# Optimization experiments

Measured on AMD Instinct MI355X. Metric: run time of the kernel, lower is better.

## Reference

```python
import jax, jax.numpy as jnp
import numpy as np

N_NODES = 50000
N_EDGES = 1600000
IN_CH = 128
HID = 64
HEADS = 2
OUT_CH2 = HID // 8  # 8
OUT_FC = 1
N_GRAPHS = 64
NEG_SLOPE = 0.2


def setup_inputs() -> dict:
    key = jax.random.key(0)
    ks = jax.random.split(key, 12)
    x = jax.random.normal(ks[0], (N_NODES, IN_CH), dtype=jnp.float32)
    edge_index = jax.random.randint(ks[1], (2, N_EDGES), 0, N_NODES, dtype=jnp.int32)
    batch = jnp.sort(jax.random.randint(ks[2], (N_NODES,), 0, N_GRAPHS, dtype=jnp.int32))
    s = lambda fan: 1.0 / np.sqrt(fan)
    W1 = jax.random.normal(ks[3], (IN_CH, HEADS * HID), dtype=jnp.float32) * s(IN_CH)
    att_src1 = jax.random.normal(ks[4], (HEADS, HID), dtype=jnp.float32) * s(HID)
    att_dst1 = jax.random.normal(ks[5], (HEADS, HID), dtype=jnp.float32) * s(HID)
    b1 = jnp.zeros((HEADS * HID,), dtype=jnp.float32)
    W2 = jax.random.normal(ks[6], (HEADS * HID, OUT_CH2), dtype=jnp.float32) * s(HEADS * HID)
    att_src2 = jax.random.normal(ks[7], (1, OUT_CH2), dtype=jnp.float32) * s(OUT_CH2)
    att_dst2 = jax.random.normal(ks[8], (1, OUT_CH2), dtype=jnp.float32) * s(OUT_CH2)
    b2 = jnp.zeros((OUT_CH2,), dtype=jnp.float32)
    fcW = jax.random.normal(ks[9], (OUT_CH2, OUT_FC), dtype=jnp.float32) * s(OUT_CH2)
    fcb = jnp.zeros((OUT_FC,), dtype=jnp.float32)
    return {"x": x, "edge_index": edge_index, "batch": batch,
            "W1": W1, "att_src1": att_src1, "att_dst1": att_dst1, "b1": b1,
            "W2": W2, "att_src2": att_src2, "att_dst2": att_dst2, "b2": b2,
            "fcW": fcW, "fcb": fcb}


def gat_conv(x, edge_index, W, att_src, att_dst, bias, heads, out_ch):
    """PyG GATConv (concat=True, add_self_loops=True, negative_slope=0.2, eval mode)."""
    n = x.shape[0]
    loop = jnp.arange(n, dtype=edge_index.dtype)
    src = jnp.concatenate([edge_index[0], loop])
    dst = jnp.concatenate([edge_index[1], loop])
    h = (x @ W).reshape(n, heads, out_ch)                 # [N,H,C]
    a_src = jnp.sum(h * att_src[None], axis=-1)           # [N,H]
    a_dst = jnp.sum(h * att_dst[None], axis=-1)           # [N,H]
    logits = jax.nn.leaky_relu(a_src[src] + a_dst[dst], NEG_SLOPE)  # [E,H]
    m = jax.ops.segment_max(logits, dst, num_segments=n)  # segment softmax over dst
    e = jnp.exp(logits - m[dst])
    denom = jax.ops.segment_sum(e, dst, num_segments=n)
    alpha = e / denom[dst]                                # [E,H]
    msg = h[src] * alpha[:, :, None]                      # [E,H,C]
    out = jax.ops.segment_sum(msg, dst, num_segments=n)   # [N,H,C]
    return out.reshape(n, heads * out_ch) + bias


def reference(x, edge_index, batch, W1, att_src1, att_dst1, b1,
              W2, att_src2, att_dst2, b2, fcW, fcb):
    h = gat_conv(x, edge_index, W1, att_src1, att_dst1, b1, HEADS, HID)
    h = jax.nn.relu(h)
    h = gat_conv(h, edge_index, W2, att_src2, att_dst2, b2, 1, OUT_CH2)
    h = jax.nn.relu(h)
    # global_mean_pool over graphs
    sums = jax.ops.segment_sum(h, batch, num_segments=N_GRAPHS)
    cnts = jax.ops.segment_sum(jnp.ones((h.shape[0],), h.dtype), batch, num_segments=N_GRAPHS)
    pooled = sums / jnp.maximum(cnts, 1.0)[:, None]       # [G, OUT_CH2]
    y = pooled @ fcW + fcb
    y = 2.0 * jax.nn.sigmoid(y) - 1.0
    return y.squeeze(-1)                                  # [G]
```

## Files before the change

kernel.cpp:

```cpp
#include <hip/hip_runtime.h>
#include <math.h>

#define MAXD 96

__device__ __forceinline__ float lrelu(float v){ return v >= 0.f ? v : 0.2f * v; }

__device__ __forceinline__ unsigned short f2bf(float f){
  unsigned u = __float_as_uint(f);
  return (unsigned short)((u + 0x7fffu + ((u >> 16) & 1u)) >> 16);
}

__global__ void countK(const int* __restrict__ dstA, int E, int ET,
                       int* __restrict__ deg8, int* __restrict__ erank, int n){
  int e = blockIdx.x * blockDim.x + threadIdx.x;
  if (e >= ET) return;
  int d = (e < E) ? dstA[e] : (e - E);
  int r = blockIdx.x & 7;
  erank[e] = atomicAdd(&deg8[r * n + d], 1);
}

__global__ void scanA(int* __restrict__ deg8, int* __restrict__ excl,
                      int* __restrict__ part, int n){
  __shared__ int s[256];
  int t = threadIdx.x;
  int i = blockIdx.x * 256 + t;
  int v = 0;
  if (i < n){
    int run = 0;
    #pragma unroll
    for (int r = 0; r < 8; ++r){
      int c = deg8[r * n + i];
      deg8[r * n + i] = run;
      run += c;
    }
    v = run;
  }
  s[t] = v;
  __syncthreads();
  for (int o = 1; o < 256; o <<= 1){
    int tv = (t >= o) ? s[t - o] : 0;
    __syncthreads();
    s[t] += tv;
    __syncthreads();
  }
  if (i < n) excl[i] = s[t] - v;
  if (t == 255) part[blockIdx.x] = s[t];
}

__global__ void scanB(int* __restrict__ part, int nb){
  __shared__ int s[256];
  int t = threadIdx.x;
  int v = (t < nb) ? part[t] : 0;
  s[t] = v;
  __syncthreads();
  for (int o = 1; o < 256; o <<= 1){
    int tv = (t >= o) ? s[t - o] : 0;
    __syncthreads();
    s[t] += tv;
    __syncthreads();
  }
  if (t < nb) part[t] = s[t] - v;
}

__global__ void scanC(int* __restrict__ off, const int* __restrict__ part, int n, int ET){
  int i = blockIdx.x * 256 + threadIdx.x;
  if (i < n) off[i] += part[blockIdx.x];
  if (i == 0) off[n] = ET;
}

__global__ void scatterK(const int* __restrict__ srcA, const int* __restrict__ dstA, int E, int ET,
                         const int* __restrict__ off, const int* __restrict__ deg8,
                         const int* __restrict__ erank, int* __restrict__ csrc, int n){
  int e = blockIdx.x * blockDim.x + threadIdx.x;
  if (e >= ET) return;
  int s, d;
  if (e < E){ s = srcA[e]; d = dstA[e]; } else { s = e - E; d = s; }
  int r = (e >> 8) & 7;
  csrc[off[d] + deg8[r * n + d] + erank[e]] = s;
}

__global__ __launch_bounds__(256, 2) void gemm1(const float* __restrict__ x, const float* __restrict__ W1,
    const float* __restrict__ attS, const float* __restrict__ attD,
    unsigned short* __restrict__ h1b, float* __restrict__ a1s, float* __restrict__ a1d, int nN){
  __shared__ float4 Ws4[128][32];
  __shared__ float4 xs4[32][32];
  int t = threadIdx.x;
  const float4* Wg = reinterpret_cast<const float4*>(W1);
  #pragma unroll
  for (int i = 0; i < 16; ++i){
    int idx = t + i * 256;
    Ws4[idx >> 5][idx & 31] = Wg[idx];
  }
  int n0 = blockIdx.x * 32;
  const float4* xg = reinterpret_cast<const float4*>(x);
  #pragma unroll
  for (int i = 0; i < 4; ++i){
    int idx = t + i * 256;
    int r = idx >> 5, c = idx & 31;
    int gn = n0 + r; if (gn >= nN) gn = nN - 1;
    xs4[r][c ^ (r & 7)] = xg[(size_t)gn * 32 + c];
  }
  __syncthreads();
  int cb = t & 15, nl = t >> 4;
  int cb2 = cb * 2;
  int c0 = cb * 8;
  int sw = nl & 7;
  float4 accA0 = make_float4(0.f,0.f,0.f,0.f), accA1 = accA0;
  float4 accB0 = accA0, accB1 = accA0;
  #pragma unroll 2
  for (int k4 = 0; k4 < 32; ++k4){
    float4 xv0 = xs4[nl][k4 ^ sw];
    float4 xv1 = xs4[nl + 16][k4 ^ sw];
    float xa[4] = {xv0.x, xv0.y, xv0.z, xv0.w};
    float xb[4] = {xv1.x, xv1.y, xv1.z, xv1.w};
    #pragma unroll
    for (int j = 0; j < 4; ++j){
      float4 wA = Ws4[4 * k4 + j][cb2];
      float4 wB = Ws4[4 * k4 + j][cb2 + 1];
      accA0.x = fmaf(xa[j], wA.x, accA0.x);
      accA0.y = fmaf(xa[j], wA.y, accA0.y);
      accA0.z = fmaf(xa[j], wA.z, accA0.z);
      accA0.w = fmaf(xa[j], wA.w, accA0.w);
      accA1.x = fmaf(xa[j], wB.x, accA1.x);
      accA1.y = fmaf(xa[j], wB.y, accA1.y);
      accA1.z = fmaf(xa[j], wB.z, accA1.z);
      accA1.w = fmaf(xa[j], wB.w, accA1.w);
      accB0.x = fmaf(xb[j], wA.x, accB0.x);
      accB0.y = fmaf(xb[j], wA.y, accB0.y);
      accB0.z = fmaf(xb[j], wA.z, accB0.z);
      accB0.w = fmaf(xb[j], wA.w, accB0.w);
      accB1.x = fmaf(xb[j], wB.x, accB1.x);
      accB1.y = fmaf(xb[j], wB.y, accB1.y);
      accB1.z = fmaf(xb[j], wB.z, accB1.z);
      accB1.w = fmaf(xb[j], wB.w, accB1.w);
    }
  }
  float4 as0 = *reinterpret_cast<const float4*>(attS + c0);
  float4 as1 = *reinterpret_cast<const float4*>(attS + c0 + 4);
  float4 ad0 = *reinterpret_cast<const float4*>(attD + c0);
  float4 ad1 = *reinterpret_cast<const float4*>(attD + c0 + 4);
  #pragma unroll
  for (int j = 0; j < 2; ++j){
    int n = n0 + nl + j * 16;
    if (n >= nN) continue;
    float4 h0 = j ? accB0 : accA0;
    float4 h1v = j ? accB1 : accA1;
    uint4 pk;
    pk.x = (unsigned)f2bf(h0.x)  | ((unsigned)f2bf(h0.y)  << 16);
    pk.y = (unsigned)f2bf(h0.z)  | ((unsigned)f2bf(h0.w)  << 16);
    pk.z = (unsigned)f2bf(h1v.x) | ((unsigned)f2bf(h1v.y) << 16);
    pk.w = (unsigned)f2bf(h1v.z) | ((unsigned)f2bf(h1v.w) << 16);
    *reinterpret_cast<uint4*>(h1b + (size_t)n * 128 + c0) = pk;
    float s = h0.x*as0.x + h0.y*as0.y + h0.z*as0.z + h0.w*as0.w
            + h1v.x*as1.x + h1v.y*as1.y + h1v.z*as1.z + h1v.w*as1.w;
    float d = h0.x*ad0.x + h0.y*ad0.y + h0.z*ad0.z + h0.w*ad0.w
            + h1v.x*ad1.x + h1v.y*ad1.y + h1v.z*ad1.z + h1v.w*ad1.w;
    s += __shfl_xor(s, 1); s += __shfl_xor(s, 2); s += __shfl_xor(s, 4);
    d += __shfl_xor(d, 1); d += __shfl_xor(d, 2); d += __shfl_xor(d, 4);
    if ((cb & 7) == 0){
      int head = cb >> 3;
      a1s[n * 2 + head] = s;
      a1d[n * 2 + head] = d;
    }
  }
}

__global__ __launch_bounds__(256) void agg1(const int* __restrict__ off, const int* __restrict__ csrc,
    const float* __restrict__ a1s, const float* __restrict__ a1d,
    const unsigned short* __restrict__ h1b, const float* __restrict__ b1,
    const float* __restrict__ W2, const float* __restrict__ attS2, const float* __restrict__ attD2,
    float* __restrict__ h2, float* __restrict__ a2s, float* __restrict__ a2d, int nN){
  __shared__ float al[4][MAXD][2];
  __shared__ int   sidx[4][MAXD];
  int t = threadIdx.x;
  int w = t >> 6, lane = t & 63;
  int n = blockIdx.x * 4 + w;
  if (n >= nN) return;
  int start = off[n], end = off[n + 1];
  int deg = end - start;
  int degc = deg < MAXD ? deg : MAXD;
  float ad0 = a1d[2 * n], ad1 = a1d[2 * n + 1];
  float ls0 = 0.f, ls1 = 0.f;
  for (int i = lane; i < degc; i += 64){
    int s = csrc[start + i];
    sidx[w][i] = s;
    float2 as = *reinterpret_cast<const float2*>(a1s + 2 * s);
    float e0 = __expf(lrelu(as.x + ad0));
    float e1 = __expf(lrelu(as.y + ad1));
    al[w][i][0] = e0; al[w][i][1] = e1;
    ls0 += e0; ls1 += e1;
  }
  #pragma unroll
  for (int o = 32; o > 0; o >>= 1){
    ls0 += __shfl_xor(ls0, o);
    ls1 += __shfl_xor(ls1, o);
  }
  float d0 = ls0, d1 = ls1;
  int c4 = (lane & 31) * 4;
  int h = c4 >> 6;
  int sub = lane >> 5;
  float4 acc = make_float4(0.f, 0.f, 0.f, 0.f);
  #pragma unroll 8
  for (int k = 0; k < degc; k += 2){
    int e = k + sub;
    bool ok = e < degc;
    int ee = ok ? e : degc - 1;
    int s = sidx[w][ee];
    float wgt = ok ? al[w][ee][h] : 0.f;
    uint2 v = *reinterpret_cast<const uint2*>(h1b + (size_t)s * 128 + c4);
    acc.x = fmaf(wgt, __uint_as_float(v.x << 16),         acc.x);
    acc.y = fmaf(wgt, __uint_as_float(v.x & 0xffff0000u), acc.y);
    acc.z = fmaf(wgt, __uint_as_float(v.y << 16),         acc.z);
    acc.w = fmaf(wgt, __uint_as_float(v.y & 0xffff0000u), acc.w);
  }
  acc.x += __shfl_xor(acc.x, 32);
  acc.y += __shfl_xor(acc.y, 32);
  acc.z += __shfl_xor(acc.z, 32);
  acc.w += __shfl_xor(acc.w, 32);
  float inv = 1.f / (h ? d1 : d0);
  float4 bb = *reinterpret_cast<const float4*>(b1 + c4);
  float oj[4];
  oj[0] = fmaxf(fmaf(acc.x, inv, bb.x), 0.f);
  oj[1] = fmaxf(fmaf(acc.y, inv, bb.y), 0.f);
  oj[2] = fmaxf(fmaf(acc.z, inv, bb.z), 0.f);
  oj[3] = fmaxf(fmaf(acc.w, inv, bb.w), 0.f);
  const float4* W2v = reinterpret_cast<const float4*>(W2);
  float p8[8] = {0.f,0.f,0.f,0.f,0.f,0.f,0.f,0.f};
  #pragma unroll
  for (int j = 0; j < 4; ++j){
    float4 wlo = W2v[(c4 + j) * 2];
    float4 whi = W2v[(c4 + j) * 2 + 1];
    p8[0] = fmaf(oj[j], wlo.x, p8[0]); p8[1] = fmaf(oj[j], wlo.y, p8[1]);
    p8[2] = fmaf(oj[j], wlo.z, p8[2]); p8[3] = fmaf(oj[j], wlo.w, p8[3]);
    p8[4] = fmaf(oj[j], whi.x, p8[4]); p8[5] = fmaf(oj[j], whi.y, p8[5]);
    p8[6] = fmaf(oj[j], whi.z, p8[6]); p8[7] = fmaf(oj[j], whi.w, p8[7]);
  }
  #pragma unroll
  for (int o = 16; o > 0; o >>= 1){
    #pragma unroll
    for (int cc = 0; cc < 8; ++cc) p8[cc] += __shfl_xor(p8[cc], o);
  }
  if (lane == 0){
    *reinterpret_cast<float4*>(h2 + (size_t)n * 8)     = make_float4(p8[0], p8[1], p8[2], p8[3]);
    *reinterpret_cast<float4*>(h2 + (size_t)n * 8 + 4) = make_float4(p8[4], p8[5], p8[6], p8[7]);
    float s2 = 0.f, dd2 = 0.f;
    #pragma unroll
    for (int cc = 0; cc < 8; ++cc){
      s2  = fmaf(p8[cc], attS2[cc], s2);
      dd2 = fmaf(p8[cc], attD2[cc], dd2);
    }
    a2s[n] = s2; a2d[n] = dd2;
  }
}

__global__ __launch_bounds__(256) void agg2(const int* __restrict__ off, const int* __restrict__ csrc,
    const float* __restrict__ a2s, const float* __restrict__ a2d,
    const float* __restrict__ h2, const float* __restrict__ b2, float* __restrict__ out2, int nN){
  __shared__ float al[4][MAXD];
  __shared__ int sidx[4][MAXD];
  int t = threadIdx.x;
  int w = t >> 6, lane = t & 63;
  int n = blockIdx.x * 4 + w;
  if (n >= nN) return;
  int start = off[n], end = off[n + 1];
  int deg = end - start, degc = deg < MAXD ? deg : MAXD;
  float ad = a2d[n];
  float ls = 0.f;
  for (int i = lane; i < degc; i += 64){
    int s = csrc[start + i];
    sidx[w][i] = s;
    float e = __expf(lrelu(a2s[s] + ad));
    al[w][i] = e;
    ls += e;
  }
  #pragma unroll
  for (int o = 32; o > 0; o >>= 1) ls += __shfl_xor(ls, o);
  float dv = ls;
  int c = lane & 7, eb = lane >> 3;
  float acc = 0.f;
  #pragma unroll 4
  for (int k = 0; k < degc; k += 8){
    int e = k + eb;
    bool ok = e < degc;
    int ee = ok ? e : degc - 1;
    float wgt = ok ? al[w][ee] : 0.f;
    acc = fmaf(wgt, h2[(size_t)sidx[w][ee] * 8 + c], acc);
  }
  acc += __shfl_xor(acc, 8);
  acc += __shfl_xor(acc, 16);
  acc += __shfl_xor(acc, 32);
  if (lane < 8) out2[(size_t)n * 8 + lane] = fmaxf(acc / dv + b2[lane], 0.f);
}

__global__ __launch_bounds__(256) void poolFC(const float* __restrict__ out2,
    const int* __restrict__ batch, const float* __restrict__ fcW,
    const float* __restrict__ fcb, float* __restrict__ out, int nN){
  __shared__ float red[256];
  int g = blockIdx.x;
  int lo = 0, hi = nN;
  while (lo < hi){ int m = (lo + hi) >> 1; if (batch[m] < g) lo = m + 1; else hi = m; }
  int s = lo;
  hi = nN;
  while (lo < hi){ int m = (lo + hi) >> 1; if (batch[m] < g + 1) lo = m + 1; else hi = m; }
  int e = lo;
  int t = threadIdx.x;
  int c = t & 7, row = t >> 3;
  float acc = 0.f;
  for (int i = s + row; i < e; i += 32) acc += out2[(size_t)i * 8 + c];
  red[t] = acc;
  __syncthreads();
  for (int o = 128; o >= 8; o >>= 1){
    if (t < o) red[t] += red[t + o];
    __syncthreads();
  }
  if (t == 0){
    float cc = fmaxf((float)(e - s), 1.0f);
    float y = fcb[0];
    #pragma unroll
    for (int c2 = 0; c2 < 8; ++c2) y += (red[c2] / cc) * fcW[c2];
    out[g] = 2.f / (1.f + expf(-y)) - 1.f;
  }
}

extern "C" void kernel_launch(void* const* d_in, const int* in_sizes, int n_in,
                              void* d_out, int out_size, void* d_ws, size_t ws_size,
                              hipStream_t stream){
  const float* x    = (const float*)d_in[0];
  const int*   ei   = (const int*)d_in[1];
  const int*   batch= (const int*)d_in[2];
  const float* W1   = (const float*)d_in[3];
  const float* aS1  = (const float*)d_in[4];
  const float* aD1  = (const float*)d_in[5];
  const float* b1   = (const float*)d_in[6];
  const float* W2   = (const float*)d_in[7];
  const float* aS2  = (const float*)d_in[8];
  const float* aD2  = (const float*)d_in[9];
  const float* b2   = (const float*)d_in[10];
  const float* fcW  = (const float*)d_in[11];
  const float* fcb  = (const float*)d_in[12];
  float* out = (float*)d_out;

  const int N  = in_sizes[0] / 128;
  const int E  = in_sizes[1] / 2;
  const int ET = E + N;
  const int G  = 64;

  const int* eiSrc = ei;
  const int* eiDst = ei + E;

  char* w = (char*)d_ws;
  size_t o = 0;
  auto alloc = [&](size_t bytes)->char*{
    o = (o + 255) & ~(size_t)255;
    char* p = w + o;
    o += bytes;
    return p;
  };
  int*   deg8   = (int*)  alloc((size_t)N * 8 * 4);
  size_t zbytes = (size_t)N * 8 * 4;
  int*   csrOff = (int*)  alloc((size_t)(N + 1) * 4);
  int*   part   = (int*)  alloc(256 * 4);
  int*   erank  = (int*)  alloc((size_t)ET * 4);
  int*   csrc   = (int*)  alloc((size_t)ET * 4);
  unsigned short* h1b = (unsigned short*)alloc((size_t)N * 128 * 2);
  float* a1s    = (float*)alloc((size_t)N * 2 * 4);
  float* a1d    = (float*)alloc((size_t)N * 2 * 4);
  float* h2     = (float*)alloc((size_t)N * 8 * 4);
  float* a2s    = (float*)alloc((size_t)N * 4);
  float* a2d    = (float*)alloc((size_t)N * 4);
  float* out2   = (float*)alloc((size_t)N * 8 * 4);
  (void)ws_size; (void)n_in; (void)out_size;

  hipMemsetAsync(deg8, 0, zbytes, stream);

  int ebl = (ET + 255) / 256;
  int nbl = (N + 255) / 256;

  countK  <<<ebl, 256, 0, stream>>>(eiDst, E, ET, deg8, erank, N);
  scanA   <<<nbl, 256, 0, stream>>>(deg8, csrOff, part, N);
  scanB   <<<1,   256, 0, stream>>>(part, nbl);
  scanC   <<<nbl, 256, 0, stream>>>(csrOff, part, N, ET);
  scatterK<<<ebl, 256, 0, stream>>>(eiSrc, eiDst, E, ET, csrOff, deg8, erank, csrc, N);

  gemm1<<<(N + 31) / 32, 256, 0, stream>>>(x, W1, aS1, aD1, h1b, a1s, a1d, N);
  agg1 <<<(N + 3) / 4, 256, 0, stream>>>(csrOff, csrc, a1s, a1d, h1b, b1, W2, aS2, aD2, h2, a2s, a2d, N);
  agg2 <<<(N + 3) / 4, 256, 0, stream>>>(csrOff, csrc, a2s, a2d, h2, b2, out2, N);
  poolFC<<<G, 256, 0, stream>>>(out2, batch, fcW, fcb, out, N);
}
```

Measured before the change: 264.3 us.

## Fuse CSR build into one cooperative kernel with register-held edge ranks

Replaces the memset, count, three scan kernels and scatter with a single cooperative-launched kernel that separates phases with grid-wide syncs. Each thread keeps its edges' destinations and atomic ranks in registers, so the erank array no longer has to be written and reread through global memory. The aggregation loop's unroll factor is also raised. The trade is several grid barriers and a fixed grid size in place of separate launches.

```diff
diff --git a/kernel.cpp b/kernel.cpp
--- a/kernel.cpp
+++ b/kernel.cpp
@@ -1,7 +1,12 @@
 #include <hip/hip_runtime.h>
+#include <hip/hip_cooperative_groups.h>
 #include <math.h>
 
+namespace cg = cooperative_groups;
+
 #define MAXD 96
+#define CSRB 1024
+#define EPT  7
 
 __device__ __forceinline__ float lrelu(float v){ return v >= 0.f ? v : 0.2f * v; }
 
@@ -10,73 +15,83 @@
   return (unsigned short)((u + 0x7fffu + ((u >> 16) & 1u)) >> 16);
 }
 
-__global__ void countK(const int* __restrict__ dstA, int E, int ET,
-                       int* __restrict__ deg8, int* __restrict__ erank, int n){
-  int e = blockIdx.x * blockDim.x + threadIdx.x;
-  if (e >= ET) return;
-  int d = (e < E) ? dstA[e] : (e - E);
-  int r = blockIdx.x & 7;
-  erank[e] = atomicAdd(&deg8[r * n + d], 1);
-}
-
-__global__ void scanA(int* __restrict__ deg8, int* __restrict__ excl,
-                      int* __restrict__ part, int n){
+__global__ __launch_bounds__(256, 4) void csrK(const int* __restrict__ srcA, const int* __restrict__ dstA,
+                                               int E, int ET, int nN,
+                                               int* __restrict__ deg8, int* __restrict__ csrOff,
+                                               int* __restrict__ part, int* __restrict__ csrc){
+  cg::grid_group grid = cg::this_grid();
   __shared__ int s[256];
-  int t = threadIdx.x;
-  int i = blockIdx.x * 256 + t;
-  int v = 0;
-  if (i < n){
-    int run = 0;
-    #pragma unroll
-    for (int r = 0; r < 8; ++r){
-      int c = deg8[r * n + i];
-      deg8[r * n + i] = run;
-      run += c;
-    }
-    v = run;
-  }
-  s[t] = v;
-  __syncthreads();
-  for (int o = 1; o < 256; o <<= 1){
-    int tv = (t >= o) ? s[t - o] : 0;
+  int t = threadIdx.x, b = blockIdx.x;
+  int gtid = b * 256 + t;
+  int r = b & 7;
+  for (int i = gtid; i < 8 * nN; i += CSRB * 256) deg8[i] = 0;
+  grid.sync();
+  int dA[EPT], rkA[EPT];
+  #pragma unroll
+  for (int j = 0; j < EPT; ++j){
+    int e = gtid + j * (CSRB * 256);
+    dA[j] = -1;
+    if (e < ET){
+      int d = (e < E) ? dstA[e] : (e - E);
+      dA[j] = d;
+      rkA[j] = atomicAdd(&deg8[r * nN + d], 1);
+    }
+  }
+  grid.sync();
+  int nbl = (nN + 255) >> 8;
+  if (b < nbl){
+    int i = b * 256 + t;
+    int v = 0;
+    if (i < nN){
+      int run = 0;
+      #pragma unroll
+      for (int rr = 0; rr < 8; ++rr){
+        int c = deg8[rr * nN + i];
+        deg8[rr * nN + i] = run;
+        run += c;
+      }
+      v = run;
+    }
+    s[t] = v;
     __syncthreads();
-    s[t] += tv;
+    for (int o = 1; o < 256; o <<= 1){
+      int tv = (t >= o) ? s[t - o] : 0;
+      __syncthreads();
+      s[t] += tv;
+      __syncthreads();
+    }
+    if (i < nN) csrOff[i] = s[t] - v;
+    if (t == 255) part[b] = s[t];
+  }
+  grid.sync();
+  if (b == 0){
+    int v = (t < nbl) ? part[t] : 0;
+    s[t] = v;
     __syncthreads();
-  }
-  if (i < n) excl[i] = s[t] - v;
-  if (t == 255) part[blockIdx.x] = s[t];
-}
-
-__global__ void scanB(int* __restrict__ part, int nb){
-  __shared__ int s[256];
-  int t = threadIdx.x;
-  int v = (t < nb) ? part[t] : 0;
-  s[t] = v;
-  __syncthreads();
-  for (int o = 1; o < 256; o <<= 1){
-    int tv = (t >= o) ? s[t - o] : 0;
-    __syncthreads();
-    s[t] += tv;
-    __syncthreads();
-  }
-  if (t < nb) part[t] = s[t] - v;
-}
-
-__global__ void scanC(int* __restrict__ off, const int* __restrict__ part, int n, int ET){
-  int i = blockIdx.x * 256 + threadIdx.x;
-  if (i < n) off[i] += part[blockIdx.x];
-  if (i == 0) off[n] = ET;
-}
-
-__global__ void scatterK(const int* __restrict__ srcA, const int* __restrict__ dstA, int E, int ET,
-                         const int* __restrict__ off, const int* __restrict__ deg8,
-                         const int* __restrict__ erank, int* __restrict__ csrc, int n){
-  int e = blockIdx.x * blockDim.x + threadIdx.x;
-  if (e >= ET) return;
-  int s, d;
-  if (e < E){ s = srcA[e]; d = dstA[e]; } else { s = e - E; d = s; }
-  int r = (e >> 8) & 7;
-  csrc[off[d] + deg8[r * n + d] + erank[e]] = s;
+    for (int o = 1; o < 256; o <<= 1){
+      int tv = (t >= o) ? s[t - o] : 0;
+      __syncthreads();
+      s[t] += tv;
+      __syncthreads();
+    }
+    if (t < nbl) part[t] = s[t] - v;
+  }
+  grid.sync();
+  if (b < nbl){
+    int i = b * 256 + t;
+    if (i < nN) csrOff[i] += part[b];
+  }
+  if (gtid == 0) csrOff[nN] = ET;
+  grid.sync();
+  #pragma unroll
+  for (int j = 0; j < EPT; ++j){
+    int e = gtid + j * (CSRB * 256);
+    if (dA[j] >= 0){
+      int src = (e < E) ? srcA[e] : (e - E);
+      int d = dA[j];
+      csrc[csrOff[d] + deg8[r * nN + d] + rkA[j]] = src;
+    }
+  }
 }
 
 __global__ __launch_bounds__(256, 2) void gemm1(const float* __restrict__ x, const float* __restrict__ W1,
@@ -200,7 +215,7 @@
   int h = c4 >> 6;
   int sub = lane >> 5;
   float4 acc = make_float4(0.f, 0.f, 0.f, 0.f);
-  #pragma unroll 8
+  #pragma unroll 16
   for (int k = 0; k < degc; k += 2){
     int e = k + sub;
     bool ok = e < degc;
@@ -345,8 +360,8 @@
   const int ET = E + N;
   const int G  = 64;
 
-  const int* eiSrc = ei;
-  const int* eiDst = ei + E;
+  int* eiSrc = (int*)ei;
+  int* eiDst = (int*)ei + E;
 
   char* w = (char*)d_ws;
   size_t o = 0;
@@ -357,10 +372,8 @@
     return p;
   };
   int*   deg8   = (int*)  alloc((size_t)N * 8 * 4);
-  size_t zbytes = (size_t)N * 8 * 4;
   int*   csrOff = (int*)  alloc((size_t)(N + 1) * 4);
   int*   part   = (int*)  alloc(256 * 4);
-  int*   erank  = (int*)  alloc((size_t)ET * 4);
   int*   csrc   = (int*)  alloc((size_t)ET * 4);
   unsigned short* h1b = (unsigned short*)alloc((size_t)N * 128 * 2);
   float* a1s    = (float*)alloc((size_t)N * 2 * 4);
@@ -371,16 +384,9 @@
   float* out2   = (float*)alloc((size_t)N * 8 * 4);
   (void)ws_size; (void)n_in; (void)out_size;
 
-  hipMemsetAsync(deg8, 0, zbytes, stream);
-
-  int ebl = (ET + 255) / 256;
-  int nbl = (N + 255) / 256;
-
-  countK  <<<ebl, 256, 0, stream>>>(eiDst, E, ET, deg8, erank, N);
-  scanA   <<<nbl, 256, 0, stream>>>(deg8, csrOff, part, N);
-  scanB   <<<1,   256, 0, stream>>>(part, nbl);
-  scanC   <<<nbl, 256, 0, stream>>>(csrOff, part, N, ET);
-  scatterK<<<ebl, 256, 0, stream>>>(eiSrc, eiDst, E, ET, csrOff, deg8, erank, csrc, N);
+  int E_ = E, ET_ = ET, N_ = N;
+  void* csrArgs[] = { &eiSrc, &eiDst, &E_, &ET_, &N_, &deg8, &csrOff, &part, &csrc };
+  hipLaunchCooperativeKernel((void*)csrK, dim3(CSRB), dim3(256), csrArgs, 0, stream);
 
   gemm1<<<(N + 31) / 32, 256, 0, stream>>>(x, W1, aS1, aD1, h1b, a1s, a1d, N);
   agg1 <<<(N + 3) / 4, 256, 0, stream>>>(csrOff, csrc, a1s, a1d, h1b, b1, W2, aS2, aD2, h2, a2s, a2d, N);
```

After: 764.3 us. 189% more time.
